# Performance work log

Measured on AMD Instinct MI355X. Metric: run time of the kernel, lower is better.

## Reference

```python
import jax, jax.numpy as jnp
import numpy as np

N = 12288   # num_nodes
D = 128     # isize
K_TOP = 31  # k + 1, per top_k(similarities, self.k + 1)


def setup_inputs() -> dict:
    key = jax.random.key(0)
    features = jax.random.normal(key, (N, D), dtype=jnp.float32)
    eye = jnp.eye(D, dtype=jnp.float32)  # param_init: weight <- I, bias <- 0
    return {
        "features": features,
        "W1": eye,
        "b1": jnp.zeros((D,), jnp.float32),
        "W2": eye,
        "b2": jnp.zeros((D,), jnp.float32),
    }


def reference(features, W1, b1, W2, b2):
    # internal_forward: Linear -> ReLU -> Linear (nlayers=2, act='relu')
    h = jax.nn.relu(features @ W1.T + b1)
    h = h @ W2.T + b2
    # F.normalize(h, dim=1, p=2) with eps=1e-12
    hn = h / jnp.maximum(jnp.linalg.norm(h, axis=1, keepdims=True), 1e-12)
    # dense N x N cosine similarity
    sim = hn @ hn.T
    # top_k: keep top (k+1) entries per row, zero elsewhere; then apply_non_linearity='relu'
    vals, idx = jax.lax.top_k(sim, K_TOP)          # [N, K_TOP]
    rows = jnp.arange(sim.shape[0])[:, None]       # [N, 1]
    # relu(sim * mask) == scatter relu(top-k values) into a zero matrix
    out = jnp.zeros_like(sim).at[rows, idx].set(jax.nn.relu(vals))
    return out
```

## Files before the change

### kernel.cpp

```cpp
#include <hip/hip_runtime.h>
#include <stdint.h>
#include <math.h>

#define NN 12288
#define DD 128
#define KTOP 31
#define TILE 128
#define GB (NN / TILE)
#define TCAND 64
#define CCAP 128

typedef __attribute__((ext_vector_type(8))) short bf16x8;
typedef __attribute__((ext_vector_type(4))) float f32x4;

__device__ __forceinline__ unsigned short f2bf(float x) {
  unsigned int u = __float_as_uint(x);
  u += 0x7fffu + ((u >> 16) & 1u);
  return (unsigned short)(u >> 16);
}

__global__ __launch_bounds__(128)
void mlp_norm_kernel(const float* __restrict__ feat,
                     const float* __restrict__ W1, const float* __restrict__ b1,
                     const float* __restrict__ W2, const float* __restrict__ b2,
                     double* __restrict__ hn64, unsigned short* __restrict__ hnb) {
  __shared__ double bufA[8][DD];
  __shared__ double bufB[8][DD];
  __shared__ double mnorm[8];
  const int t = threadIdx.x;
  const int row0 = blockIdx.x * 8;

  #pragma unroll
  for (int rr = 0; rr < 8; ++rr)
    bufA[rr][t] = (double)feat[(size_t)(row0 + rr) * DD + t];
  __syncthreads();

  {
    double acc[8] = {0,0,0,0,0,0,0,0};
    const float* wrow = W1 + (size_t)t * DD;
    for (int k = 0; k < DD; ++k) {
      double w = (double)wrow[k];
      #pragma unroll
      for (int rr = 0; rr < 8; ++rr)
        acc[rr] = fma(w, bufA[rr][k], acc[rr]);
    }
    double bb = (double)b1[t];
    #pragma unroll
    for (int rr = 0; rr < 8; ++rr)
      bufB[rr][t] = fmax(acc[rr] + bb, 0.0);
  }
  __syncthreads();
  {
    double acc[8] = {0,0,0,0,0,0,0,0};
    const float* wrow = W2 + (size_t)t * DD;
    for (int k = 0; k < DD; ++k) {
      double w = (double)wrow[k];
      #pragma unroll
      for (int rr = 0; rr < 8; ++rr)
        acc[rr] = fma(w, bufB[rr][k], acc[rr]);
    }
    double bb = (double)b2[t];
    #pragma unroll
    for (int rr = 0; rr < 8; ++rr)
      bufA[rr][t] = acc[rr] + bb;
  }
  __syncthreads();

  const int lane = t & 63;
  const int w = t >> 6;
  #pragma unroll
  for (int r2 = 0; r2 < 4; ++r2) {
    int rr = w * 4 + r2;
    double x0 = bufA[rr][lane];
    double x1 = bufA[rr][lane + 64];
    double s = x0 * x0 + x1 * x1;
    #pragma unroll
    for (int d = 1; d < 64; d <<= 1)
      s += __shfl_xor(s, d);
    if (lane == 0) mnorm[rr] = fmax(sqrt(s), 1e-12);
  }
  __syncthreads();
  #pragma unroll
  for (int rr = 0; rr < 8; ++rr) {
    double v = bufA[rr][t] / mnorm[rr];
    hn64[(size_t)(row0 + rr) * DD + t] = v;
    hnb[(size_t)(row0 + rr) * DD + t] = f2bf((float)v);
  }
}

__device__ __forceinline__ int lunit(int c, int r, int q) {
  return c * 512 + r * 4 + ((q + (r >> 1)) & 3);
}

__global__ __launch_bounds__(256)
void gemm_kernel(const unsigned short* __restrict__ hnb,
                 unsigned short* __restrict__ simmat) {
  __shared__ __attribute__((aligned(16))) unsigned short At[16384];
  __shared__ __attribute__((aligned(16))) unsigned short Bt[16384];
  const int t = threadIdx.x;
  const int lane = t & 63;
  const int wv = t >> 6;
  const int bi = blockIdx.x / GB, bj = blockIdx.x % GB;
  const int r0 = bi * TILE, c0 = bj * TILE;

  #pragma unroll
  for (int i = 0; i < 8; ++i) {
    int u = i * 256 + t;
    int c = u >> 9, r = (u >> 2) & 127, g = u & 3;
    int q = (g - (r >> 1)) & 3;
    uint4 v = *(const uint4*)(hnb + (size_t)(r0 + r) * DD + c * 32 + q * 8);
    *(uint4*)(At + u * 8) = v;
  }
  #pragma unroll
  for (int i = 0; i < 8; ++i) {
    int u = i * 256 + t;
    int c = u >> 9, r = (u >> 2) & 127, g = u & 3;
    int q = (g - (r >> 1)) & 3;
    uint4 v = *(const uint4*)(hnb + (size_t)(c0 + r) * DD + c * 32 + q * 8);
    *(uint4*)(Bt + u * 8) = v;
  }
  __syncthreads();

  const int wr = (wv >> 1) * 64;
  const int wc = (wv & 1) * 64;
  const int m = lane & 15, quad = lane >> 4;

  f32x4 acc[4][4] = {};
  #pragma unroll
  for (int kc = 0; kc < 4; ++kc) {
    bf16x8 a[4], b[4];
    #pragma unroll
    for (int i = 0; i < 4; ++i)
      a[i] = *(const bf16x8*)(At + lunit(kc, wr + i * 16 + m, quad) * 8);
    #pragma unroll
    for (int j = 0; j < 4; ++j)
      b[j] = *(const bf16x8*)(Bt + lunit(kc, wc + j * 16 + m, quad) * 8);
    #pragma unroll
    for (int i = 0; i < 4; ++i)
      #pragma unroll
      for (int j = 0; j < 4; ++j)
        acc[i][j] = __builtin_amdgcn_mfma_f32_16x16x32_bf16(a[i], b[j], acc[i][j], 0, 0, 0);
  }

  const bool evenl = !(lane & 1);
  #pragma unroll
  for (int i = 0; i < 4; ++i)
    #pragma unroll
    for (int j = 0; j < 4; ++j)
      #pragma unroll
      for (int r = 0; r < 4; ++r) {
        float v = acc[i][j][r];
        float v2 = __shfl_xor(v, 1);
        if (evenl) {
          unsigned int pk = (unsigned int)f2bf(v) | ((unsigned int)f2bf(v2) << 16);
          int R = r0 + wr + i * 16 + quad * 4 + r;
          int C = c0 + wc + j * 16 + m;
          *(unsigned int*)(simmat + (size_t)R * NN + C) = pk;
        }
      }
}

#define PINS(P) { \
  unsigned p_ = (P); \
  _Pragma("unroll") \
  for (int i_ = 0; i_ < 7; ++i_) \
    L[i_] = (p_ > L[i_ + 1]) ? L[i_ + 1] : (L[i_] > p_ ? L[i_] : p_); \
  L[7] = L[7] > p_ ? L[7] : p_; }

__global__ __launch_bounds__(256)
void scan_rescore_kernel(const unsigned short* __restrict__ simmat,
                         const double* __restrict__ hn64,
                         float* __restrict__ resval, int* __restrict__ rescol) {
  __shared__ unsigned scand[4][CCAP];
  const int t = threadIdx.x, lane = t & 63, wv = t >> 6;
  const int row = blockIdx.x * 4 + wv;
  const unsigned short* srow = simmat + (size_t)row * NN;

  unsigned L[8] = {0, 0, 0, 0, 0, 0, 0, 0};
  for (int it = 0; it < NN / 512; ++it) {
    uint4 pk = *(const uint4*)(srow + it * 512 + lane * 8);
    const unsigned cb = it * 512 + lane * 8;
    unsigned wds[4] = {pk.x, pk.y, pk.z, pk.w};
    #pragma unroll
    for (int q = 0; q < 4; ++q) {
      unsigned b0 = wds[q] & 0xFFFFu, b1 = wds[q] >> 16;
      unsigned s0 = (b0 & 0x8000u) ? 0u : b0;
      unsigned s1 = (b1 & 0x8000u) ? 0u : b1;
      unsigned p0 = (s0 << 16) | (cb + 2 * q);
      unsigned p1 = (s1 << 16) | (cb + 2 * q + 1);
      if (p0 > L[0]) { PINS(p0) }
      if (p1 > L[0]) { PINS(p1) }
    }
  }

  unsigned lo = 0, hi = 0xFFFFu;
  while (lo < hi) {
    unsigned mid = (lo + hi + 1) >> 1;
    int c = 0;
    #pragma unroll
    for (int i = 0; i < 8; ++i) c += (int)((L[i] >> 16) >= mid);
    #pragma unroll
    for (int d = 1; d < 64; d <<= 1) c += __shfl_xor(c, d);
    if (c >= TCAND) lo = mid; else hi = mid - 1;
  }
  const unsigned thr = lo;

  int cl = 0;
  #pragma unroll
  for (int i = 0; i < 8; ++i) cl += (int)((L[i] >> 16) >= thr);
  int pre = cl;
  #pragma unroll
  for (int d = 1; d < 64; d <<= 1) {
    int y = __shfl_up(pre, d);
    if (lane >= d) pre += y;
  }
  const int total = __shfl(pre, 63);
  const int nc = total < CCAP ? total : CCAP;
  int slot = pre - cl;
  #pragma unroll
  for (int i = 0; i < 8; ++i) {
    if ((L[i] >> 16) >= thr) {
      if (slot < CCAP) scand[wv][slot] = L[i];
      ++slot;
    }
  }
  __syncthreads();

  const double* arow = hn64 + (size_t)row * DD;
  double rv0 = -1.0e300, rv1 = -1.0e300;
  int rc0 = 0x7fffffff, rc1 = 0x7fffffff;
  if (lane < nc) {
    const int col = (int)(scand[wv][lane] & 0xFFFFu);
    const double* brow = hn64 + (size_t)col * DD;
    double acc = 0.0;
    for (int k = 0; k < DD; k += 2) {
      double2 a2 = *(const double2*)(arow + k);
      double2 b2 = *(const double2*)(brow + k);
      acc = fma(a2.x, b2.x, acc);
      acc = fma(a2.y, b2.y, acc);
    }
    rv0 = acc; rc0 = col;
  }
  if (lane + 64 < nc) {
    const int col = (int)(scand[wv][lane + 64] & 0xFFFFu);
    const double* brow = hn64 + (size_t)col * DD;
    double acc = 0.0;
    for (int k = 0; k < DD; k += 2) {
      double2 a2 = *(const double2*)(arow + k);
      double2 b2 = *(const double2*)(brow + k);
      acc = fma(a2.x, b2.x, acc);
      acc = fma(a2.y, b2.y, acc);
    }
    rv1 = acc; rc1 = col;
  }

  for (int itk = 0; itk < KTOP; ++itk) {
    bool f = (rv0 > rv1) || (rv0 == rv1 && rc0 < rc1);
    double bv = f ? rv0 : rv1;
    int bc = f ? rc0 : rc1;
    #pragma unroll
    for (int d = 1; d < 64; d <<= 1) {
      double ov = __shfl_xor(bv, d);
      int    oc = __shfl_xor(bc, d);
      bool tk = (ov > bv) || (ov == bv && oc < bc);
      bv = tk ? ov : bv;
      bc = tk ? oc : bc;
    }
    if (lane == itk) {
      resval[(size_t)row * KTOP + itk] = (float)fmax(bv, 0.0);
      rescol[(size_t)row * KTOP + itk] = bc;
    }
    if (rv0 == bv && rc0 == bc) rv0 = -1.0e300;
    else if (rv1 == bv && rc1 == bc) rv1 = -1.0e300;
  }
}

__global__ __launch_bounds__(256)
void emit_kernel(const float* __restrict__ resval, const int* __restrict__ rescol,
                 float* __restrict__ out) {
  const int row = blockIdx.x, t = threadIdx.x;
  float v = 0.0f; int c = 0;
  if (t < KTOP) {
    v = resval[(size_t)row * KTOP + t];
    c = rescol[(size_t)row * KTOP + t];
  }
  float4* orow = (float4*)(out + (size_t)row * NN);
  const float4 z = {0.0f, 0.0f, 0.0f, 0.0f};
  #pragma unroll
  for (int i = 0; i < NN / 4 / 256; ++i)
    orow[i * 256 + t] = z;
  __syncthreads();
  if (t < KTOP) out[(size_t)row * NN + c] = v;
}

extern "C" void kernel_launch(void* const* d_in, const int* in_sizes, int n_in,
                              void* d_out, int out_size, void* d_ws, size_t ws_size,
                              hipStream_t stream) {
  const float* feat = (const float*)d_in[0];
  const float* W1 = (const float*)d_in[1];
  const float* b1 = (const float*)d_in[2];
  const float* W2 = (const float*)d_in[3];
  const float* b2 = (const float*)d_in[4];
  float* out = (float*)d_out;

  double* hn64 = (double*)d_ws;
  unsigned short* hnb = (unsigned short*)(hn64 + (size_t)NN * DD);
  float* resval = (float*)(hnb + (size_t)NN * DD);
  int* rescol = (int*)(resval + (size_t)NN * KTOP);

  unsigned short* simmat = (unsigned short*)d_out;

  mlp_norm_kernel<<<NN / 8, 128, 0, stream>>>(feat, W1, b1, W2, b2, hn64, hnb);
  gemm_kernel<<<GB * GB, 256, 0, stream>>>(hnb, simmat);
  scan_rescore_kernel<<<NN / 4, 256, 0, stream>>>(simmat, hn64, resval, rescol);
  emit_kernel<<<NN, 256, 0, stream>>>(resval, rescol, out);
}
```

Measured before the change: 1.025 ms.

## Fuse output zeroing for the first half of rows into scan kernel, transpose MLP weights

The bf16 similarity matrix now lives in the second half of the output buffer, so the scan kernel can zero and scatter the first 6144 output rows directly without clobbering data it still has to read. Only the remaining rows go through the emit kernel. Output zeroing uses nontemporal stores. The top-8 insertion uses v_med3_u32 unconditionally instead of a guarded branch. A small kernel transposes W1/W2 so the MLP reads weights coalesced with paired LDS loads. This cuts one pass of output writes and relieves branch divergence, at the cost of an extra launch and unconditional insertion work per element.

After: 1.016 ms. About the same (-0.9%).

```diff
diff --git a/kernel.cpp b/kernel.cpp
--- a/kernel.cpp
+++ b/kernel.cpp
@@ -9,6 +9,7 @@
 #define GB (NN / TILE)
 #define TCAND 64
 #define CCAP 128
+#define FUSE_ROWS 6144
 
 typedef __attribute__((ext_vector_type(8))) short bf16x8;
 typedef __attribute__((ext_vector_type(4))) float f32x4;
@@ -19,10 +20,24 @@
   return (unsigned short)(u >> 16);
 }
 
+__device__ __forceinline__ unsigned umed3(unsigned a, unsigned b, unsigned c) {
+  unsigned d;
+  asm("v_med3_u32 %0, %1, %2, %3" : "=v"(d) : "v"(a), "v"(b), "v"(c));
+  return d;
+}
+
+__global__ __launch_bounds__(128)
+void wtrans_kernel(const float* __restrict__ W1, const float* __restrict__ W2,
+                   float* __restrict__ W1T, float* __restrict__ W2T) {
+  const int r = blockIdx.x, c = threadIdx.x;
+  W1T[(size_t)c * DD + r] = W1[(size_t)r * DD + c];
+  W2T[(size_t)c * DD + r] = W2[(size_t)r * DD + c];
+}
+
 __global__ __launch_bounds__(128)
 void mlp_norm_kernel(const float* __restrict__ feat,
-                     const float* __restrict__ W1, const float* __restrict__ b1,
-                     const float* __restrict__ W2, const float* __restrict__ b2,
+                     const float* __restrict__ W1T, const float* __restrict__ b1,
+                     const float* __restrict__ W2T, const float* __restrict__ b2,
                      double* __restrict__ hn64, unsigned short* __restrict__ hnb) {
   __shared__ double bufA[8][DD];
   __shared__ double bufB[8][DD];
@@ -37,12 +52,15 @@
 
   {
     double acc[8] = {0,0,0,0,0,0,0,0};
-    const float* wrow = W1 + (size_t)t * DD;
-    for (int k = 0; k < DD; ++k) {
-      double w = (double)wrow[k];
+    for (int k = 0; k < DD; k += 2) {
+      double w0 = (double)W1T[(size_t)k * DD + t];
+      double w1 = (double)W1T[(size_t)(k + 1) * DD + t];
       #pragma unroll
-      for (int rr = 0; rr < 8; ++rr)
-        acc[rr] = fma(w, bufA[rr][k], acc[rr]);
+      for (int rr = 0; rr < 8; ++rr) {
+        double2 a2 = *(const double2*)(&bufA[rr][k]);
+        acc[rr] = fma(w0, a2.x, acc[rr]);
+        acc[rr] = fma(w1, a2.y, acc[rr]);
+      }
     }
     double bb = (double)b1[t];
     #pragma unroll
@@ -52,12 +70,15 @@
   __syncthreads();
   {
     double acc[8] = {0,0,0,0,0,0,0,0};
-    const float* wrow = W2 + (size_t)t * DD;
-    for (int k = 0; k < DD; ++k) {
-      double w = (double)wrow[k];
+    for (int k = 0; k < DD; k += 2) {
+      double w0 = (double)W2T[(size_t)k * DD + t];
+      double w1 = (double)W2T[(size_t)(k + 1) * DD + t];
       #pragma unroll
-      for (int rr = 0; rr < 8; ++rr)
-        acc[rr] = fma(w, bufB[rr][k], acc[rr]);
+      for (int rr = 0; rr < 8; ++rr) {
+        double2 a2 = *(const double2*)(&bufB[rr][k]);
+        acc[rr] = fma(w0, a2.x, acc[rr]);
+        acc[rr] = fma(w1, a2.y, acc[rr]);
+      }
     }
     double bb = (double)b2[t];
     #pragma unroll
@@ -161,16 +182,17 @@
 }
 
 #define PINS(P) { \
-  unsigned p_ = (P); \
+  const unsigned p_ = (P); \
   _Pragma("unroll") \
   for (int i_ = 0; i_ < 7; ++i_) \
-    L[i_] = (p_ > L[i_ + 1]) ? L[i_ + 1] : (L[i_] > p_ ? L[i_] : p_); \
+    L[i_] = umed3(p_, L[i_], L[i_ + 1]); \
   L[7] = L[7] > p_ ? L[7] : p_; }
 
 __global__ __launch_bounds__(256)
 void scan_rescore_kernel(const unsigned short* __restrict__ simmat,
                          const double* __restrict__ hn64,
-                         float* __restrict__ resval, int* __restrict__ rescol) {
+                         float* __restrict__ resval, int* __restrict__ rescol,
+                         float* __restrict__ out) {
   __shared__ unsigned scand[4][CCAP];
   const int t = threadIdx.x, lane = t & 63, wv = t >> 6;
   const int row = blockIdx.x * 4 + wv;
@@ -183,13 +205,13 @@
     unsigned wds[4] = {pk.x, pk.y, pk.z, pk.w};
     #pragma unroll
     for (int q = 0; q < 4; ++q) {
-      unsigned b0 = wds[q] & 0xFFFFu, b1 = wds[q] >> 16;
+      unsigned b0 = wds[q] & 0xFFFFu, b1v = wds[q] >> 16;
       unsigned s0 = (b0 & 0x8000u) ? 0u : b0;
-      unsigned s1 = (b1 & 0x8000u) ? 0u : b1;
+      unsigned s1 = (b1v & 0x8000u) ? 0u : b1v;
       unsigned p0 = (s0 << 16) | (cb + 2 * q);
       unsigned p1 = (s1 << 16) | (cb + 2 * q + 1);
-      if (p0 > L[0]) { PINS(p0) }
-      if (p1 > L[0]) { PINS(p1) }
+      PINS(p0)
+      PINS(p1)
     }
   }
 
@@ -254,6 +276,8 @@
     rv1 = acc; rc1 = col;
   }
 
+  const bool fuse = (row < FUSE_ROWS);
+  float fkv = 0.0f; int fkc = 0;
   for (int itk = 0; itk < KTOP; ++itk) {
     bool f = (rv0 > rv1) || (rv0 == rv1 && rc0 < rc1);
     double bv = f ? rv0 : rv1;
@@ -267,28 +291,42 @@
       bc = tk ? oc : bc;
     }
     if (lane == itk) {
-      resval[(size_t)row * KTOP + itk] = (float)fmax(bv, 0.0);
-      rescol[(size_t)row * KTOP + itk] = bc;
+      float ovv = (float)fmax(bv, 0.0);
+      fkv = ovv; fkc = bc;
+      if (!fuse) {
+        resval[(size_t)row * KTOP + itk] = ovv;
+        rescol[(size_t)row * KTOP + itk] = bc;
+      }
     }
     if (rv0 == bv && rc0 == bc) rv0 = -1.0e300;
     else if (rv1 == bv && rc1 == bc) rv1 = -1.0e300;
+  }
+
+  if (fuse) {
+    f32x4* orow = (f32x4*)(out + (size_t)row * NN);
+    const f32x4 z = {0.0f, 0.0f, 0.0f, 0.0f};
+    #pragma unroll
+    for (int i = 0; i < NN / 4 / 64; ++i)
+      __builtin_nontemporal_store(z, &orow[i * 64 + lane]);
+    __syncthreads();
+    if (lane < KTOP) out[(size_t)row * NN + fkc] = fkv;
   }
 }
 
 __global__ __launch_bounds__(256)
 void emit_kernel(const float* __restrict__ resval, const int* __restrict__ rescol,
                  float* __restrict__ out) {
-  const int row = blockIdx.x, t = threadIdx.x;
+  const int row = blockIdx.x + FUSE_ROWS, t = threadIdx.x;
   float v = 0.0f; int c = 0;
   if (t < KTOP) {
     v = resval[(size_t)row * KTOP + t];
     c = rescol[(size_t)row * KTOP + t];
   }
-  float4* orow = (float4*)(out + (size_t)row * NN);
-  const float4 z = {0.0f, 0.0f, 0.0f, 0.0f};
+  f32x4* orow = (f32x4*)(out + (size_t)row * NN);
+  const f32x4 z = {0.0f, 0.0f, 0.0f, 0.0f};
   #pragma unroll
   for (int i = 0; i < NN / 4 / 256; ++i)
-    orow[i * 256 + t] = z;
+    __builtin_nontemporal_store(z, &orow[i * 256 + t]);
   __syncthreads();
   if (t < KTOP) out[(size_t)row * NN + c] = v;
 }
@@ -307,11 +345,14 @@
   unsigned short* hnb = (unsigned short*)(hn64 + (size_t)NN * DD);
   float* resval = (float*)(hnb + (size_t)NN * DD);
   int* rescol = (int*)(resval + (size_t)NN * KTOP);
-
-  unsigned short* simmat = (unsigned short*)d_out;
-
-  mlp_norm_kernel<<<NN / 8, 128, 0, stream>>>(feat, W1, b1, W2, b2, hn64, hnb);
+  float* W1T = (float*)(rescol + (size_t)NN * KTOP);
+  float* W2T = W1T + DD * DD;
+
+  unsigned short* simmat = (unsigned short*)((char*)d_out + (size_t)NN * NN * 2);
+
+  wtrans_kernel<<<DD, DD, 0, stream>>>(W1, W2, W1T, W2T);
+  mlp_norm_kernel<<<NN / 8, 128, 0, stream>>>(feat, W1T, b1, W2T, b2, hn64, hnb);
   gemm_kernel<<<GB * GB, 256, 0, stream>>>(hnb, simmat);
-  scan_rescore_kernel<<<NN / 4, 256, 0, stream>>>(simmat, hn64, resval, rescol);
-  emit_kernel<<<NN, 256, 0, stream>>>(resval, rescol, out);
-}
+  scan_rescore_kernel<<<NN / 4, 256, 0, stream>>>(simmat, hn64, resval, rescol, out);
+  emit_kernel<<<NN - FUSE_ROWS, 256, 0, stream>>>(resval, rescol, out);
+}
```
